# Performance work log

Hardware: AMD Instinct MI355X
Metric: run time of the kernel (lower is better)

The kernel has to match this reference:

```python
import jax, jax.numpy as jnp
import numpy as np

NUM_LEVELS = 4
RADIUS = 4


def setup_inputs() -> dict:
    key = jax.random.key(0)
    k1, k2, k3 = jax.random.split(key, 3)
    B, C, H, W = 2, 256, 64, 64
    N = 4
    fmap1 = jax.random.normal(k1, (B, C, H, W), dtype=jnp.float32)
    fmap2 = jax.random.normal(k2, (B, C, H, W), dtype=jnp.float32)
    # coords channel 0 = x in [0, W-1], channel 1 = y in [0, H-1]
    coords = jax.random.uniform(k3, (B, N, 2, H, W), dtype=jnp.float32) * (W - 1)
    return {"fmap1": fmap1, "fmap2": fmap2, "coords": coords}


def _bilinear_gather(corr, x, y):
    """Zero-padded bilinear sampling (grid_sample align_corners=True semantics).
    corr: (B, P, h2, w2) per-query-pixel correlation maps.
    x, y: (B, N, P, K2) absolute pixel coords into (w2, h2).
    Returns (B, N, P, K2)."""
    Bv, P, h2, w2 = corr.shape
    x0 = jnp.floor(x)
    y0 = jnp.floor(y)
    wx1 = x - x0
    wy1 = y - y0
    b = jnp.arange(Bv)[:, None, None, None]
    p = jnp.arange(P)[None, None, :, None]

    def corner(yi, xi):
        valid = (xi >= 0) & (xi <= w2 - 1) & (yi >= 0) & (yi <= h2 - 1)
        xi_c = jnp.clip(xi, 0, w2 - 1).astype(jnp.int32)
        yi_c = jnp.clip(yi, 0, h2 - 1).astype(jnp.int32)
        v = corr[b, p, yi_c, xi_c]
        return jnp.where(valid, v, jnp.zeros((), corr.dtype))

    v00 = corner(y0, x0)
    v01 = corner(y0, x0 + 1)
    v10 = corner(y0 + 1, x0)
    v11 = corner(y0 + 1, x0 + 1)
    return ((1 - wy1) * (1 - wx1) * v00 + (1 - wy1) * wx1 * v01
            + wy1 * (1 - wx1) * v10 + wy1 * wx1 * v11)


def reference(fmap1, fmap2, coords):
    B, C, H, W = fmap1.shape
    _, N = coords.shape[0], coords.shape[1]
    P = H * W
    r = RADIUS
    K = 2 * r + 1
    K2 = K * K

    # All-pairs correlation: (B, P_query, H2, W2), scaled by 1/sqrt(C) (RAFT)
    f1 = fmap1.reshape(B, C, P)
    f2 = fmap2.reshape(B, C, P)
    corr = jnp.einsum('bcp,bcq->bpq', f1, f2) / jnp.sqrt(jnp.asarray(C, fmap1.dtype))
    corr = corr.reshape(B, P, H, W)

    # Pyramid via 2x2 average pooling (stride 2, no padding)
    pyramid = [corr]
    c = corr
    for _ in range(NUM_LEVELS - 1):
        h2, w2 = c.shape[-2:]
        c = c.reshape(B, P, h2 // 2, 2, w2 // 2, 2).mean(axis=(3, 5))
        pyramid.append(c)

    # Window offsets. Faithful to the torch code: delta = stack(meshgrid(dy, dx, 'ij'))
    # so delta[...,0] = yy is added to the x-channel, delta[...,1] = xx to the y-channel.
    d = jnp.linspace(-r, r, K).astype(coords.dtype)
    yy, xx = jnp.meshgrid(d, d, indexing='ij')
    off_x = yy.reshape(1, 1, 1, K2)  # added to coords[...,0]
    off_y = xx.reshape(1, 1, 1, K2)  # added to coords[...,1]

    cx = coords[:, :, 0].reshape(B, N, P)  # (B, N, P)
    cy = coords[:, :, 1].reshape(B, N, P)

    outs = []
    for i, cl in enumerate(pyramid):
        scale = jnp.asarray(2.0 ** i, coords.dtype)
        x = cx[..., None] / scale + off_x  # (B, N, P, K2)
        y = cy[..., None] / scale + off_y
        v = _bilinear_gather(cl, x, y)     # (B, N, P, K2)
        outs.append(v.reshape(B, N, H, W, K2))

    out = jnp.concatenate(outs, axis=-1)   # (B, N, H, W, L*K2)
    Ctot = out.shape[-1]
    # Matches torch: contiguous (B,N,H,W,C) reshaped row-major to (B, N*C, H, W)
    out = out.reshape(B, N * Ctot, H, W)
    return out.astype(jnp.float32)
```

## Files before the change

kernel.cpp:

```cpp
#include <hip/hip_runtime.h>
#include <hip/hip_bf16.h>
#include <cstdint>

#define B_    2
#define C_    256
#define H_    64
#define W_    64
#define P_    (H_*W_)
#define N_    4
#define RAD   4
#define K2_   81
#define CTOT  (4*K2_)

typedef __bf16 bf16x8 __attribute__((ext_vector_type(8)));
typedef float  f32x4  __attribute__((ext_vector_type(4)));

__device__ __forceinline__ void gload_lds16(const void* g, void* l) {
    __builtin_amdgcn_global_load_lds(
        (const __attribute__((address_space(1))) void*)g,
        (__attribute__((address_space(3))) void*)l,
        16, 0, 0);
}

__global__ void transpose_cvt(const float* __restrict__ in0,
                              const float* __restrict__ in1,
                              __hip_bfloat16* __restrict__ out0,
                              __hip_bfloat16* __restrict__ out1) {
    __shared__ float tile[32][33];
    const int z     = blockIdx.z;
    const int which = z >> 1;
    const int b     = z & 1;
    const float* in          = which ? in1  : in0;
    __hip_bfloat16* out      = which ? out1 : out0;
    const int p0 = blockIdx.x * 32;
    const int c0 = blockIdx.y * 32;
    const int tx = threadIdx.x;
    const int ty = threadIdx.y;
    const float* src = in + ((size_t)b * C_ + c0) * P_ + p0;
    #pragma unroll
    for (int i = 0; i < 32; i += 8)
        tile[ty + i][tx] = src[(size_t)(ty + i) * P_ + tx];
    __syncthreads();
    __hip_bfloat16* dst = out + ((size_t)b * P_ + p0) * C_ + c0;
    #pragma unroll
    for (int i = 0; i < 32; i += 8)
        dst[(size_t)(ty + i) * C_ + tx] = __float2bfloat16(tile[tx][ty + i]);
}

#define TSTR 136

__global__ __launch_bounds__(256) void gemm_corr(
    const short* __restrict__ f1t,
    const short* __restrict__ f2t,
    __hip_bfloat16* __restrict__ corr0,
    __hip_bfloat16* __restrict__ corr1)
{
    __shared__ short smem[32768];

    const int tid  = threadIdx.x;
    const int lane = tid & 63;
    const int wv   = tid >> 6;
    const int wm   = (wv >> 1) * 64;
    const int wn   = (wv & 1) * 64;
    const int b    = blockIdx.z;
    const int bx   = blockIdx.x;
    const int m0   = blockIdx.y * 128;
    const int n0   = bx * 128;
    const int qd   = lane >> 4;
    const int l15  = lane & 15;

    const short* gA[4];
    const short* gB[4];
    int ldsOff[4];
    #pragma unroll
    for (int it = 0; it < 4; ++it) {
        const int ci = it * 256 + tid;
        const int r  = ci >> 3;
        const int cp = ci & 7;
        const int kc = cp ^ (r & 7);
        gA[it] = f1t + ((size_t)(b * P_ + m0 + r)) * C_ + kc * 8;
        gB[it] = f2t + ((size_t)(b * P_ + n0 + r)) * C_ + kc * 8;
        ldsOff[it] = (it * 256 + wv * 64) * 8;
    }

    int aAddr[4][2], bAddr[4][2];
    #pragma unroll
    for (int i = 0; i < 4; ++i) {
        const int m = wm + i * 16 + l15;
        const int n = wn + i * 16 + l15;
        #pragma unroll
        for (int s = 0; s < 2; ++s) {
            const int lc = s * 4 + qd;
            aAddr[i][s] = m * 64 + ((lc ^ (m & 7)) * 8);
            bAddr[i][s] = n * 64 + ((lc ^ (n & 7)) * 8);
        }
    }

    f32x4 zero = {0.f, 0.f, 0.f, 0.f};
    f32x4 acc[4][4];
    #pragma unroll
    for (int mi = 0; mi < 4; ++mi)
        #pragma unroll
        for (int ni = 0; ni < 4; ++ni)
            acc[mi][ni] = zero;

    #pragma unroll
    for (int it = 0; it < 4; ++it) {
        gload_lds16(gA[it], smem + ldsOff[it]);
        gload_lds16(gB[it], smem + 8192 + ldsOff[it]);
    }

    #pragma unroll
    for (int kt = 0; kt < 4; ++kt) {
        __syncthreads();
        if (kt < 3) {
            const int nxt = ((kt + 1) & 1) * 16384;
            const int k0  = (kt + 1) * 64;
            #pragma unroll
            for (int it = 0; it < 4; ++it) {
                gload_lds16(gA[it] + k0, smem + nxt + ldsOff[it]);
                gload_lds16(gB[it] + k0, smem + nxt + 8192 + ldsOff[it]);
            }
        }
        const short* As = smem + (kt & 1) * 16384;
        const short* Bs = As + 8192;
        #pragma unroll
        for (int s = 0; s < 2; ++s) {
            bf16x8 af[4], bfr[4];
            #pragma unroll
            for (int i = 0; i < 4; ++i) {
                af[i]  = *(const bf16x8*)(As + aAddr[i][s]);
                bfr[i] = *(const bf16x8*)(Bs + bAddr[i][s]);
            }
            #pragma unroll
            for (int mi = 0; mi < 4; ++mi)
                #pragma unroll
                for (int ni = 0; ni < 4; ++ni)
                    acc[mi][ni] = __builtin_amdgcn_mfma_f32_16x16x32_bf16(
                        af[mi], bfr[ni], acc[mi][ni], 0, 0, 0);
        }
    }
    __syncthreads();

    const float sc = 0.0625f;
    __hip_bfloat16* tile = (__hip_bfloat16*)smem;
    #pragma unroll
    for (int mi = 0; mi < 4; ++mi) {
        #pragma unroll
        for (int ni = 0; ni < 4; ++ni) {
            #pragma unroll
            for (int r = 0; r < 4; ++r) {
                const int rl = wm + mi * 16 + qd * 4 + r;
                const int cl = wn + ni * 16 + l15;
                tile[rl * TSTR + cl] = __float2bfloat16(acc[mi][ni][r] * sc);
            }
        }
    }
    __syncthreads();

    #pragma unroll
    for (int i = 0; i < 8; ++i) {
        const int cid = i * 256 + tid;
        const int tr  = cid >> 4;
        const int tc  = cid & 15;
        const float4 v = *(const float4*)(smem + tr * TSTR + tc * 8);
        *(float4*)(corr0 + ((size_t)(b * P_ + m0 + tr)) * P_ + n0 + tc * 8) = v;
    }

    #pragma unroll
    for (int i = 0; i < 16; ++i) {
        const int oid = i * 256 + tid;
        const int pr  = oid >> 5;
        const int pc  = oid & 31;
        const uint32_t u0 = *(const uint32_t*)(smem + pr * TSTR + 2 * pc);
        const uint32_t u1 = *(const uint32_t*)(smem + pr * TSTR + 64 + 2 * pc);
        const float a0 = __uint_as_float(u0 << 16);
        const float a1 = __uint_as_float(u0 & 0xffff0000u);
        const float b0 = __uint_as_float(u1 << 16);
        const float b1 = __uint_as_float(u1 & 0xffff0000u);
        corr1[((size_t)(b * P_ + m0 + pr)) * 1024 + bx * 32 + pc] =
            __float2bfloat16((a0 + a1 + b0 + b1) * 0.25f);
    }
}

__global__ __launch_bounds__(256) void gather4(
    const float* __restrict__ coords,
    const __hip_bfloat16* __restrict__ c0,
    const __hip_bfloat16* __restrict__ c1,
    float* __restrict__ out) {
    __shared__ float pool_sm[320];
    __shared__ float patch[4][440];
    __shared__ int   gsm[4][8];
    __shared__ float wsm[4][4][4];

    const int tid  = threadIdx.x;
    const int lane = tid & 63;
    const int n    = tid >> 6;
    const int bp   = blockIdx.x;
    const int b    = bp >> 12;
    const int p    = bp & (P_ - 1);

    const __hip_bfloat16* c0b = c0 + (size_t)bp * 4096;
    const __hip_bfloat16* c1b = c1 + (size_t)bp * 1024;

    {
        const int y2 = tid >> 4, x2 = tid & 15;
        const uint32_t u0 = *(const uint32_t*)(c1b + (2 * y2) * 32 + 2 * x2);
        const uint32_t u1 = *(const uint32_t*)(c1b + (2 * y2 + 1) * 32 + 2 * x2);
        const float a0 = __uint_as_float(u0 << 16);
        const float a1 = __uint_as_float(u0 & 0xffff0000u);
        const float b0 = __uint_as_float(u1 << 16);
        const float b1 = __uint_as_float(u1 & 0xffff0000u);
        pool_sm[tid] = (a0 + a1 + b0 + b1) * 0.25f;
    }
    __syncthreads();
    if (tid < 64) {
        const int y3 = tid >> 3, x3 = tid & 7;
        const float* r0 = pool_sm + (2 * y3) * 16 + 2 * x3;
        pool_sm[256 + tid] = (r0[0] + r0[1] + r0[16] + r0[17]) * 0.25f;
    }
    __syncthreads();

    const float cx = coords[((size_t)((b * N_ + n) * 2 + 0)) * P_ + p];
    const float cy = coords[((size_t)((b * N_ + n) * 2 + 1)) * P_ + p];
    if (lane < 4) {
        const int l = lane;
        const float inv = (l == 0) ? 1.f : (l == 1) ? 0.5f : (l == 2) ? 0.25f : 0.125f;
        const float x = cx * inv, y = cy * inv;
        const float x0f = floorf(x), y0f = floorf(y);
        const float wx = x - x0f, wy = y - y0f;
        gsm[n][l]     = (int)x0f - RAD;
        gsm[n][4 + l] = (int)y0f - RAD;
        wsm[n][l][0] = (1.f - wy) * (1.f - wx);
        wsm[n][l][1] = (1.f - wy) * wx;
        wsm[n][l][2] = wy * (1.f - wx);
        wsm[n][l][3] = wy * wx;
    }

    float* pw = patch[n];

    #pragma unroll
    for (int lvl = 0; lvl < 2; ++lvl) {
        const __hip_bfloat16* src = lvl ? c1b : c0b;
        const int hw = lvl ? 32 : 64;
        const int sh = lvl ? 5 : 6;
        const int xb = gsm[n][lvl];
        const int yb = gsm[n][4 + lvl];
        #pragma unroll
        for (int it = 0; it < 2; ++it) {
            const int idx = it * 64 + lane;
            if (idx < 110) {
                const int r  = idx / 11;
                const int cc = idx - r * 11;
                const int gr = yb + r, gc = xb + cc;
                float v = 0.f;
                if ((cc < 10) & ((unsigned)gr < (unsigned)hw) &
                    ((unsigned)gc < (unsigned)hw))
                    v = __bfloat162float(src[(gr << sh) + gc]);
                pw[lvl * 110 + idx] = v;
            }
        }
    }
    #pragma unroll
    for (int lvl = 2; lvl < 4; ++lvl) {
        const int hw   = (lvl == 2) ? 16 : 8;
        const int sh   = (lvl == 2) ? 4 : 3;
        const int base = (lvl == 2) ? 0 : 256;
        const int xb = gsm[n][lvl];
        const int yb = gsm[n][4 + lvl];
        #pragma unroll
        for (int it = 0; it < 2; ++it) {
            const int idx = it * 64 + lane;
            if (idx < 110) {
                const int r  = idx / 11;
                const int cc = idx - r * 11;
                const int gr = yb + r, gc = xb + cc;
                float v = 0.f;
                if ((cc < 10) & ((unsigned)gr < (unsigned)hw) &
                    ((unsigned)gc < (unsigned)hw))
                    v = pool_sm[base + (gr << sh) + gc];
                pw[lvl * 110 + idx] = v;
            }
        }
    }

    const size_t obase = ((size_t)(b * N_ + n) * P_ + p) * CTOT;
    #pragma unroll
    for (int it = 0; it < 6; ++it) {
        const int o = it * 64 + lane;
        if (o < CTOT) {
            const int lvl = o / K2_;
            const int k2  = o - lvl * K2_;
            const int ki  = k2 / 9;
            const int kj  = k2 - ki * 9;
            const float4 w = *(const float4*)&wsm[n][lvl][0];
            const float* pr = pw + lvl * 110 + kj * 11 + ki;
            out[obase + o] = w.x * pr[0] + w.y * pr[1] +
                             w.z * pr[11] + w.w * pr[12];
        }
    }
}

extern "C" void kernel_launch(void* const* d_in, const int* in_sizes, int n_in,
                              void* d_out, int out_size, void* d_ws, size_t ws_size,
                              hipStream_t stream) {
    const float* fmap1  = (const float*)d_in[0];
    const float* fmap2  = (const float*)d_in[1];
    const float* coords = (const float*)d_in[2];
    float* out = (float*)d_out;

    char* ws = (char*)d_ws;
    __hip_bfloat16* f1t = (__hip_bfloat16*)ws;
    __hip_bfloat16* f2t = (__hip_bfloat16*)(ws + 4194304);
    __hip_bfloat16* c0  = (__hip_bfloat16*)(ws + 8388608);
    __hip_bfloat16* c1  = (__hip_bfloat16*)(ws + 75497472);

    {
        dim3 grid(P_ / 32, C_ / 32, 2 * B_);
        dim3 blk(32, 8);
        transpose_cvt<<<grid, blk, 0, stream>>>(fmap1, fmap2, f1t, f2t);
    }

    {
        dim3 grid(P_ / 128, P_ / 128, B_);
        gemm_corr<<<grid, 256, 0, stream>>>((const short*)f1t, (const short*)f2t,
                                            c0, c1);
    }

    gather4<<<B_ * P_, 256, 0, stream>>>(coords, c0, c1, out);
}
```

Measured before the change: 129.9 us.

## Single-buffer GEMM LDS and hoist gather coord math and loads ahead of pooling

The correlation GEMM drops its double-buffered LDS prefetch and uses a single buffer with load-then-sync per k-step, shrinking shared memory from 64KB to about 34KB so more blocks can fit per CU. In exchange, global-to-LDS loads no longer overlap the MFMA work. The gather kernel now computes the per-level bilinear coordinates and weights redundantly in every lane, removing the shared-memory weight/index arrays and a dependency on lane<4. It also issues the level 0/1 global reads before the pooling barrier to hide their latency, and splits the output loop per level to avoid divides.

Result: faster. 122.6 us (-5.6%).

```diff
diff --git a/kernel.cpp b/kernel.cpp
--- a/kernel.cpp
+++ b/kernel.cpp
@@ -55,7 +55,9 @@
     __hip_bfloat16* __restrict__ corr0,
     __hip_bfloat16* __restrict__ corr1)
 {
-    __shared__ short smem[32768];
+    __shared__ short smem[128 * TSTR];
+    short* As = smem;
+    short* Bs = smem + 8192;
 
     const int tid  = threadIdx.x;
     const int lane = tid & 63;
@@ -104,26 +106,14 @@
         for (int ni = 0; ni < 4; ++ni)
             acc[mi][ni] = zero;
 
-    #pragma unroll
-    for (int it = 0; it < 4; ++it) {
-        gload_lds16(gA[it], smem + ldsOff[it]);
-        gload_lds16(gB[it], smem + 8192 + ldsOff[it]);
-    }
-
-    #pragma unroll
     for (int kt = 0; kt < 4; ++kt) {
+        const int k0 = kt * 64;
+        #pragma unroll
+        for (int it = 0; it < 4; ++it) {
+            gload_lds16(gA[it] + k0, As + ldsOff[it]);
+            gload_lds16(gB[it] + k0, Bs + ldsOff[it]);
+        }
         __syncthreads();
-        if (kt < 3) {
-            const int nxt = ((kt + 1) & 1) * 16384;
-            const int k0  = (kt + 1) * 64;
-            #pragma unroll
-            for (int it = 0; it < 4; ++it) {
-                gload_lds16(gA[it] + k0, smem + nxt + ldsOff[it]);
-                gload_lds16(gB[it] + k0, smem + nxt + 8192 + ldsOff[it]);
-            }
-        }
-        const short* As = smem + (kt & 1) * 16384;
-        const short* Bs = As + 8192;
         #pragma unroll
         for (int s = 0; s < 2; ++s) {
             bf16x8 af[4], bfr[4];
@@ -139,8 +129,8 @@
                     acc[mi][ni] = __builtin_amdgcn_mfma_f32_16x16x32_bf16(
                         af[mi], bfr[ni], acc[mi][ni], 0, 0, 0);
         }
-    }
-    __syncthreads();
+        __syncthreads();
+    }
 
     const float sc = 0.0625f;
     __hip_bfloat16* tile = (__hip_bfloat16*)smem;
@@ -183,15 +173,13 @@
     }
 }
 
-__global__ __launch_bounds__(256) void gather4(
+__global__ __launch_bounds__(256) void gather5(
     const float* __restrict__ coords,
     const __hip_bfloat16* __restrict__ c0,
     const __hip_bfloat16* __restrict__ c1,
     float* __restrict__ out) {
     __shared__ float pool_sm[320];
     __shared__ float patch[4][440];
-    __shared__ int   gsm[4][8];
-    __shared__ float wsm[4][4][4];
 
     const int tid  = threadIdx.x;
     const int lane = tid & 63;
@@ -202,6 +190,44 @@
 
     const __hip_bfloat16* c0b = c0 + (size_t)bp * 4096;
     const __hip_bfloat16* c1b = c1 + (size_t)bp * 1024;
+
+    const float cx = coords[((size_t)((b * N_ + n) * 2 + 0)) * P_ + p];
+    const float cy = coords[((size_t)((b * N_ + n) * 2 + 1)) * P_ + p];
+    int x0i[4], y0i[4];
+    float w00[4], w01[4], w10[4], w11[4];
+    #pragma unroll
+    for (int l = 0; l < 4; ++l) {
+        const float inv = (l == 0) ? 1.f : (l == 1) ? 0.5f : (l == 2) ? 0.25f : 0.125f;
+        const float x = cx * inv, y = cy * inv;
+        const float x0f = floorf(x), y0f = floorf(y);
+        const float wx = x - x0f, wy = y - y0f;
+        x0i[l] = (int)x0f - RAD;
+        y0i[l] = (int)y0f - RAD;
+        w00[l] = (1.f - wy) * (1.f - wx);
+        w01[l] = (1.f - wy) * wx;
+        w10[l] = wy * (1.f - wx);
+        w11[l] = wy * wx;
+    }
+
+    float pv[2][2];
+    #pragma unroll
+    for (int lvl = 0; lvl < 2; ++lvl) {
+        const __hip_bfloat16* src = lvl ? c1b : c0b;
+        const int hw = lvl ? 32 : 64;
+        const int sh = lvl ? 5 : 6;
+        #pragma unroll
+        for (int it = 0; it < 2; ++it) {
+            const int idx = it * 64 + lane;
+            const int r   = idx / 11;
+            const int cc  = idx - r * 11;
+            const int gr  = y0i[lvl] + r, gc = x0i[lvl] + cc;
+            float v = 0.f;
+            if ((idx < 110) & (cc < 10) & ((unsigned)gr < (unsigned)hw) &
+                ((unsigned)gc < (unsigned)hw))
+                v = __bfloat162float(src[(gr << sh) + gc]);
+            pv[lvl][it] = v;
+        }
+    }
 
     {
         const int y2 = tid >> 4, x2 = tid & 15;
@@ -221,60 +247,27 @@
     }
     __syncthreads();
 
-    const float cx = coords[((size_t)((b * N_ + n) * 2 + 0)) * P_ + p];
-    const float cy = coords[((size_t)((b * N_ + n) * 2 + 1)) * P_ + p];
-    if (lane < 4) {
-        const int l = lane;
-        const float inv = (l == 0) ? 1.f : (l == 1) ? 0.5f : (l == 2) ? 0.25f : 0.125f;
-        const float x = cx * inv, y = cy * inv;
-        const float x0f = floorf(x), y0f = floorf(y);
-        const float wx = x - x0f, wy = y - y0f;
-        gsm[n][l]     = (int)x0f - RAD;
-        gsm[n][4 + l] = (int)y0f - RAD;
-        wsm[n][l][0] = (1.f - wy) * (1.f - wx);
-        wsm[n][l][1] = (1.f - wy) * wx;
-        wsm[n][l][2] = wy * (1.f - wx);
-        wsm[n][l][3] = wy * wx;
-    }
-
     float* pw = patch[n];
-
     #pragma unroll
     for (int lvl = 0; lvl < 2; ++lvl) {
-        const __hip_bfloat16* src = lvl ? c1b : c0b;
-        const int hw = lvl ? 32 : 64;
-        const int sh = lvl ? 5 : 6;
-        const int xb = gsm[n][lvl];
-        const int yb = gsm[n][4 + lvl];
+        #pragma unroll
+        for (int it = 0; it < 2; ++it) {
+            const int idx = it * 64 + lane;
+            if (idx < 110) pw[lvl * 110 + idx] = pv[lvl][it];
+        }
+    }
+    #pragma unroll
+    for (int lvl = 2; lvl < 4; ++lvl) {
+        const int hw   = (lvl == 2) ? 16 : 8;
+        const int sh   = (lvl == 2) ? 4 : 3;
+        const int base = (lvl == 2) ? 0 : 256;
         #pragma unroll
         for (int it = 0; it < 2; ++it) {
             const int idx = it * 64 + lane;
             if (idx < 110) {
                 const int r  = idx / 11;
                 const int cc = idx - r * 11;
-                const int gr = yb + r, gc = xb + cc;
-                float v = 0.f;
-                if ((cc < 10) & ((unsigned)gr < (unsigned)hw) &
-                    ((unsigned)gc < (unsigned)hw))
-                    v = __bfloat162float(src[(gr << sh) + gc]);
-                pw[lvl * 110 + idx] = v;
-            }
-        }
-    }
-    #pragma unroll
-    for (int lvl = 2; lvl < 4; ++lvl) {
-        const int hw   = (lvl == 2) ? 16 : 8;
-        const int sh   = (lvl == 2) ? 4 : 3;
-        const int base = (lvl == 2) ? 0 : 256;
-        const int xb = gsm[n][lvl];
-        const int yb = gsm[n][4 + lvl];
-        #pragma unroll
-        for (int it = 0; it < 2; ++it) {
-            const int idx = it * 64 + lane;
-            if (idx < 110) {
-                const int r  = idx / 11;
-                const int cc = idx - r * 11;
-                const int gr = yb + r, gc = xb + cc;
+                const int gr = y0i[lvl] + r, gc = x0i[lvl] + cc;
                 float v = 0.f;
                 if ((cc < 10) & ((unsigned)gr < (unsigned)hw) &
                     ((unsigned)gc < (unsigned)hw))
@@ -286,17 +279,19 @@
 
     const size_t obase = ((size_t)(b * N_ + n) * P_ + p) * CTOT;
     #pragma unroll
-    for (int it = 0; it < 6; ++it) {
-        const int o = it * 64 + lane;
-        if (o < CTOT) {
-            const int lvl = o / K2_;
-            const int k2  = o - lvl * K2_;
-            const int ki  = k2 / 9;
-            const int kj  = k2 - ki * 9;
-            const float4 w = *(const float4*)&wsm[n][lvl][0];
-            const float* pr = pw + lvl * 110 + kj * 11 + ki;
-            out[obase + o] = w.x * pr[0] + w.y * pr[1] +
-                             w.z * pr[11] + w.w * pr[12];
+    for (int lvl = 0; lvl < 4; ++lvl) {
+        const float* pl = pw + lvl * 110;
+        float* ol = out + obase + lvl * K2_;
+        #pragma unroll
+        for (int it = 0; it < 2; ++it) {
+            const int k2 = it * 64 + lane;
+            if (k2 < K2_) {
+                const int ki = k2 / 9;
+                const int kj = k2 - ki * 9;
+                const float* pr = pl + kj * 11 + ki;
+                ol[k2] = w00[lvl] * pr[0] + w01[lvl] * pr[1] +
+                         w10[lvl] * pr[11] + w11[lvl] * pr[12];
+            }
         }
     }
 }
@@ -327,5 +322,5 @@
                                             c0, c1);
     }
 
-    gather4<<<B_ * P_, 256, 0, stream>>>(coords, c0, c1, out);
-}
+    gather5<<<B_ * P_, 256, 0, stream>>>(coords, c0, c1, out);
+}
```
